# Optimization experiments

Measured on AMD Instinct MI355X. Metric: run time of the kernel, lower is better.

Reference implementation:

```python
import jax, jax.numpy as jnp
import numpy as np

NUM_HEADS = 8
HEAD_DIM = 64
LATENT = NUM_HEADS * HEAD_DIM  # 512
IN_CH = 256


def setup_inputs() -> dict:
    key = jax.random.key(0)
    k1, k2, k3, k4 = jax.random.split(key, 4)
    b, c, h, w = 16, IN_CH, 64, 64
    net = jax.random.normal(k1, (b, c, h, w), dtype=jnp.float32)
    # 1x1 conv weights (out_ch, in_ch); scaled like kaiming-ish init
    w_qkv = jax.random.normal(k2, (3 * LATENT, c), dtype=jnp.float32) / np.sqrt(c)
    w_out = jax.random.normal(k3, (c, LATENT), dtype=jnp.float32) / np.sqrt(LATENT)
    b_out = jax.random.normal(k4, (c,), dtype=jnp.float32) * 0.01
    return {"net": net, "w_qkv": w_qkv, "w_out": w_out, "b_out": b_out}


def reference(net, w_qkv, w_out, b_out):
    b, c, h, w = net.shape
    n = h * w
    # 1x1 conv == channel GEMM: (b, 3L, n)
    qkv = jnp.einsum("bchw,oc->bohw", net, w_qkv).reshape(b, 3, NUM_HEADS, HEAD_DIM, n)
    q, k, v = qkv[:, 0], qkv[:, 1], qkv[:, 2]  # each (b, H, D, n)
    k = jax.nn.softmax(k, axis=-1)  # softmax over spatial tokens
    context = jnp.einsum("bhdn,bhen->bhde", k, v)  # (b, H, D, D)
    out = jnp.einsum("bhde,bhdn->bhen", context, q)  # (b, H, D, n)
    out = out.reshape(b, LATENT, h, w)
    # output 1x1 conv with bias
    out = jnp.einsum("blhw,cl->bchw", out, w_out) + b_out[None, :, None, None]
    return out
```

## Files before the change

### kernel.cpp

```cpp
#include <hip/hip_runtime.h>


typedef unsigned short u16;
typedef unsigned int u32;
typedef __attribute__((ext_vector_type(4))) u16 u16x4;
typedef __attribute__((ext_vector_type(4))) u32 u32x4;
typedef __attribute__((ext_vector_type(4))) float f32x4;
typedef __attribute__((ext_vector_type(8))) short bf16x8;

__device__ __forceinline__ u16 f2bf(float f) {
  union { float f; u32 u; } x; x.f = f;
  u32 r = x.u + 0x7fffu + ((x.u >> 16) & 1u);
  return (u16)(r >> 16);
}

__device__ __forceinline__ void async16(const u16* g, u16* l) {
  __builtin_amdgcn_global_load_lds(
      (const __attribute__((address_space(1))) void*)g,
      (__attribute__((address_space(3))) void*)l, 16, 0, 0);
}

__global__ __launch_bounds__(256) void prep_all(const float* __restrict__ net,
                                                u16* __restrict__ netT,
                                                const float* __restrict__ wqkv,
                                                u16* __restrict__ wkv,
                                                u16* __restrict__ wqTb) {
  __shared__ float t[64][65];
  const int blk = blockIdx.x;
  const int tid = threadIdx.x;
  if (blk < 4096) {
    const int b = blk >> 8, c0 = ((blk >> 6) & 3) * 64, n0 = (blk & 63) * 64;
    const float* ip = net + (size_t)b * 256 * 4096;
    u16* op = netT + (size_t)b * 256 * 4096;
    const int col4 = (tid & 15) * 4, rr0 = tid >> 4;
#pragma unroll
    for (int i = 0; i < 4; ++i) {
      int r = rr0 + i * 16;
      f32x4 v = *(const f32x4*)(ip + (size_t)(c0 + r) * 4096 + n0 + col4);
      t[r][col4 + 0] = v[0]; t[r][col4 + 1] = v[1];
      t[r][col4 + 2] = v[2]; t[r][col4 + 3] = v[3];
    }
    __syncthreads();
    const int c8 = (tid & 7) * 8, nr0 = tid >> 3;
#pragma unroll
    for (int i = 0; i < 2; ++i) {
      int nr = nr0 + i * 32;
      u16 tmp[8];
#pragma unroll
      for (int k = 0; k < 8; ++k) tmp[k] = f2bf(t[c8 + k][nr]);
      *(u32x4*)(op + (size_t)(n0 + nr) * 256 + c0 + c8) = *(const u32x4*)tmp;
    }
  } else if (blk < 4352) {
    const float* w = wqkv + 512 * 256;
    int i = ((blk - 4096) * 256 + tid) * 4;
    f32x4 v = *(const f32x4*)(w + i);
    u16x4 u;
    u[0] = f2bf(v[0]); u[1] = f2bf(v[1]); u[2] = f2bf(v[2]); u[3] = f2bf(v[3]);
    *(u16x4*)(wkv + i) = u;
  } else {
    const int idx = blk - 4352;
    const int c0 = (idx & 3) * 64, r0 = (idx >> 2) * 64;
    const int col4 = (tid & 15) * 4, rr0 = tid >> 4;
#pragma unroll
    for (int i = 0; i < 4; ++i) {
      int r = rr0 + i * 16;
      f32x4 v = *(const f32x4*)(wqkv + (size_t)(r0 + r) * 256 + c0 + col4);
      t[r][col4 + 0] = v[0]; t[r][col4 + 1] = v[1];
      t[r][col4 + 2] = v[2]; t[r][col4 + 3] = v[3];
    }
    __syncthreads();
    const int cc4 = (tid & 15) * 4, nr0 = tid >> 4;
#pragma unroll
    for (int i = 0; i < 4; ++i) {
      int nr = nr0 + i * 16;
      u16x4 u;
      u[0] = f2bf(t[cc4 + 0][nr]); u[1] = f2bf(t[cc4 + 1][nr]);
      u[2] = f2bf(t[cc4 + 2][nr]); u[3] = f2bf(t[cc4 + 3][nr]);
      *(u16x4*)(wqTb + (size_t)(c0 + nr) * 512 + r0 + cc4) = u;
    }
  }
}

__global__ __launch_bounds__(512, 4) void kv_ctx_fused(
    const u16* __restrict__ wkv,
    const u16* __restrict__ netT,
    float* __restrict__ ctxp,
    float* __restrict__ sump) {
  __shared__ __align__(16) u16 Bs[2][8192];
  __shared__ __align__(16) u16 ekL[2][2048];
  __shared__ __align__(16) u16 vL[2][2048];

  const int flat = blockIdx.x;
  const int xcd = flat & 7, inner = flat >> 3;
  const int b = 2 * xcd + (inner >> 5);
  const int h = (inner >> 2) & 7;
  const int s = inner & 3;

  const int tid = threadIdx.x, lane = tid & 63, wid = tid >> 6;
  const int wq = wid & 3, wn = wid >> 2;
  const int lr = lane & 15, lg = lane >> 4;
  const bool isK = (wq < 2);

  bf16x8 af[2][8];
#pragma unroll
  for (int mi = 0; mi < 2; ++mi) {
    const int r = wq * 32 + mi * 16 + lr;
    const int grow = (r < 64) ? h * 64 + r : 512 + h * 64 + (r - 64);
#pragma unroll
    for (int kk = 0; kk < 8; ++kk)
      af[mi][kk] = *(const bf16x8*)(wkv + (size_t)grow * 256 + kk * 32 + lg * 8);
  }

  const u16* Bsrc = netT + ((size_t)b * 4096 + s * 1024) * 256;
  const int srow = tid >> 5;
  const int sslot = tid & 31;
  auto stage = [&](int c, int buf) {
    const u16* src = Bsrc + (size_t)c * 32 * 256;
#pragma unroll
    for (int i = 0; i < 2; ++i) {
      const int row = i * 16 + srow;
      const int scol = ((sslot ^ (row & 7)) * 8);
      async16(src + row * 256 + scol, &Bs[buf][i * 4096 + tid * 8]);
    }
  };

  f32x4 cacc[2] = {};
  f32x4 sacc = {};
  bf16x8 ones8;
#pragma unroll
  for (int j = 0; j < 8; ++j) ((u16*)&ones8)[j] = 0x3F80;

  auto ctx_acc = [&](int q) {
    const int d = wq * 16 + lr;
    bf16x8 ekf = *(const bf16x8*)&ekL[q][d * 32 + ((lg ^ (d & 3)) * 8)];
#pragma unroll
    for (int ei = 0; ei < 2; ++ei) {
      const int e = wn * 32 + ei * 16 + lr;
      bf16x8 vf = *(const bf16x8*)&vL[q][e * 32 + ((lg ^ (e & 3)) * 8)];
      cacc[ei] = __builtin_amdgcn_mfma_f32_16x16x32_bf16(ekf, vf, cacc[ei], 0, 0, 0);
    }
    if (wn == 0)
      sacc = __builtin_amdgcn_mfma_f32_16x16x32_bf16(ekf, ones8, sacc, 0, 0, 0);
  };

  stage(0, 0);
  const int nrow = wn * 16 + lr;

  for (int c = 0; c < 32; ++c) {
    const int p = c & 1;
    __syncthreads();
    if (c + 1 < 32) stage(c + 1, p ^ 1);

    f32x4 kvacc[2] = {};
    __builtin_amdgcn_s_setprio(1);
    if (c > 0) ctx_acc(p ^ 1);
#pragma unroll
    for (int kk = 0; kk < 8; ++kk) {
      bf16x8 bfr = *(const bf16x8*)&Bs[p][nrow * 256 + (((kk * 4 + lg) ^ (nrow & 7)) * 8)];
      kvacc[0] = __builtin_amdgcn_mfma_f32_16x16x32_bf16(af[0][kk], bfr, kvacc[0], 0, 0, 0);
      kvacc[1] = __builtin_amdgcn_mfma_f32_16x16x32_bf16(af[1][kk], bfr, kvacc[1], 0, 0, 0);
    }
    __builtin_amdgcn_s_setprio(0);

    u16* dstL = isK ? ekL[p] : vL[p];
#pragma unroll
    for (int mi = 0; mi < 2; ++mi)
#pragma unroll
      for (int j = 0; j < 4; ++j) {
        float v = kvacc[mi][j];
        if (isK) v = __expf(v);
        const u32 u = __float_as_uint(v);
        const u16 bv = (u16)((u + 0x8000u) >> 16);
        const int dd = (wq & 1) * 32 + mi * 16 + lg * 4 + j;
        dstL[dd * 32 + (((nrow >> 3) ^ (dd & 3)) * 8) + (nrow & 7)] = bv;
      }
  }
  __syncthreads();
  ctx_acc(1);

  float* cp = ctxp + (((size_t)(b * 8 + h) * 4 + s) * 4096);
#pragma unroll
  for (int ei = 0; ei < 2; ++ei)
#pragma unroll
    for (int j = 0; j < 4; ++j) {
      const int d = wq * 16 + lg * 4 + j;
      const int e = wn * 32 + ei * 16 + lr;
      cp[d * 64 + e] = cacc[ei][j];
    }
  if (wn == 0 && lr == 0) {
#pragma unroll
    for (int j = 0; j < 4; ++j)
      sump[((size_t)(b * 8 + h) * 4 + s) * 64 + wq * 16 + lg * 4 + j] = sacc[j];
  }
}

__global__ __launch_bounds__(256) void fold_w2(const float* __restrict__ ctxp,
                                               const float* __restrict__ sump,
                                               const float* __restrict__ wout,
                                               u16* __restrict__ W2) {
  __shared__ float cl[16 * 64];
  __shared__ float sl[16];
  const int bh = blockIdx.x, dq = blockIdx.y;
  const int b = bh >> 3, h = bh & 7;
  const int tid = threadIdx.x;
  f32x4 v4 = {0.f, 0.f, 0.f, 0.f};
#pragma unroll
  for (int ch = 0; ch < 4; ++ch)
    v4 += *(const f32x4*)(ctxp + ((size_t)bh * 4 + ch) * 4096 + dq * 1024 + tid * 4);
  *(f32x4*)&cl[tid * 4] = v4;
  if (tid < 16) {
    float ss = 0.f;
#pragma unroll
    for (int ch = 0; ch < 4; ++ch)
      ss += sump[((size_t)bh * 4 + ch) * 64 + dq * 16 + tid];
    sl[tid] = ss;
  }
  __syncthreads();
  const int c = tid;
  f32x4 wv[16];
  const float* wrow = wout + (size_t)c * 512 + h * 64;
#pragma unroll
  for (int i = 0; i < 16; ++i) wv[i] = *(const f32x4*)(wrow + i * 4);
#pragma unroll
  for (int d = 0; d < 16; ++d) {
    f32x4 s4 = {0.f, 0.f, 0.f, 0.f};
#pragma unroll
    for (int e4 = 0; e4 < 16; ++e4) {
      f32x4 cv = *(const f32x4*)&cl[d * 64 + e4 * 4];
      s4 += wv[e4] * cv;
    }
    const float s = (s4[0] + s4[1] + s4[2] + s4[3]) / sl[d];
    W2[((size_t)b * 256 + c) * 512 + h * 64 + dq * 16 + d] = f2bf(s);
  }
}

template <int LD, int NK, int MODE>
__global__ __launch_bounds__(256) void gemm128(const u16* __restrict__ A,
                                               const u16* __restrict__ B,
                                               size_t aStride, size_t bStride,
                                               void* __restrict__ O0,
                                               const float* __restrict__ bias) {
  __shared__ __align__(16) u16 SM[32768];
  int b, mt, nt;
  if constexpr (MODE == 1) {
    const int flat = blockIdx.x;
    const int xcd = flat & 7, r = flat >> 3;
    b = 2 * xcd + (r >> 6);
    nt = (r & 63) >> 1;
    mt = r & 1;
  } else {
    b = blockIdx.z; mt = blockIdx.y; nt = blockIdx.x;
  }
  const int tid = threadIdx.x, lane = tid & 63, wid = tid >> 6;
  const int wr = wid >> 1, wc = wid & 1, lr = lane & 15, lg = lane >> 4;
  const u16* Ap = A + (size_t)b * aStride + (size_t)mt * 128 * LD;
  const u16* Bp = B + (size_t)b * bStride + (size_t)nt * 128 * LD;

  auto stage = [&](int buf, int ks) {
    const int k0 = ks * 64;
#pragma unroll
    for (int i = 0; i < 4; ++i) {
      const int idx = i * 2048 + tid * 8;
      const int r2 = idx >> 6, c2 = idx & 63;
      async16(Ap + (size_t)r2 * LD + k0 + c2, SM + buf * 8192 + i * 2048 + wid * 512);
      async16(Bp + (size_t)r2 * LD + k0 + c2, SM + 16384 + buf * 8192 + i * 2048 + wid * 512);
    }
  };

  f32x4 acc[4][4] = {};
  stage(0, 0);
  asm volatile("s_waitcnt vmcnt(0)" ::: "memory");
  __syncthreads();
  for (int ks = 0; ks < NK; ++ks) {
    const int buf = ks & 1;
    if (ks + 1 < NK) stage(buf ^ 1, ks + 1);
    const u16* Ab = SM + buf * 8192;
    const u16* Bb = SM + 16384 + buf * 8192;
#pragma unroll
    for (int kk = 0; kk < 2; ++kk) {
      bf16x8 afm[4], bfr[4];
#pragma unroll
      for (int mi = 0; mi < 4; ++mi)
        afm[mi] = *(const bf16x8*)(Ab + (wr * 64 + mi * 16 + lr) * 64 + kk * 32 + lg * 8);
#pragma unroll
      for (int ni = 0; ni < 4; ++ni)
        bfr[ni] = *(const bf16x8*)(Bb + (wc * 64 + ni * 16 + lr) * 64 + kk * 32 + lg * 8);
#pragma unroll
      for (int mi = 0; mi < 4; ++mi)
#pragma unroll
        for (int ni = 0; ni < 4; ++ni)
          acc[mi][ni] = __builtin_amdgcn_mfma_f32_16x16x32_bf16(afm[mi], bfr[ni], acc[mi][ni], 0, 0, 0);
    }
    asm volatile("s_waitcnt vmcnt(0)" ::: "memory");
    __syncthreads();
  }

  if constexpr (MODE == 2) {
    u16* Cs = SM;
#pragma unroll
    for (int mi = 0; mi < 4; ++mi)
#pragma unroll
      for (int ni = 0; ni < 4; ++ni)
#pragma unroll
        for (int j = 0; j < 4; ++j)
          Cs[(wr * 64 + mi * 16 + lg * 4 + j) * 128 + wc * 64 + ni * 16 + lr] =
              f2bf(acc[mi][ni][j]);
    __syncthreads();
    u16* dst = (u16*)O0;
#pragma unroll
    for (int p = 0; p < 8; ++p) {
      const int idx = p * 2048 + tid * 8;
      const int r2 = idx >> 7, cc = idx & 127;
      *(u32x4*)(dst + ((size_t)b * 256 + mt * 128 + r2) * 256 + nt * 128 + cc) =
          *(const u32x4*)(Cs + idx);
    }
  } else {
    float* Cf = (float*)SM;
#pragma unroll
    for (int mi = 0; mi < 4; ++mi)
#pragma unroll
      for (int ni = 0; ni < 4; ++ni)
#pragma unroll
        for (int j = 0; j < 4; ++j) {
          const int row = wr * 64 + mi * 16 + lg * 4 + j;
          Cf[row * 128 + wc * 64 + ni * 16 + lr] = acc[mi][ni][j] + bias[mt * 128 + row];
        }
    __syncthreads();
    float* op = (float*)O0;
#pragma unroll
    for (int p = 0; p < 16; ++p) {
      const int idx = p * 1024 + tid * 4;
      const int r2 = idx >> 7, cc = idx & 127;
      *(f32x4*)(op + ((size_t)b * 256 + mt * 128 + r2) * 4096 + nt * 128 + cc) =
          *(const f32x4*)(Cf + idx);
    }
  }
}

extern "C" void kernel_launch(void* const* d_in, const int* in_sizes, int n_in,
                              void* d_out, int out_size, void* d_ws, size_t ws_size,
                              hipStream_t stream) {
  const float* net  = (const float*)d_in[0];
  const float* wqkv = (const float*)d_in[1];
  const float* wout = (const float*)d_in[2];
  const float* bout = (const float*)d_in[3];
  float* out = (float*)d_out;

  char* ws = (char*)d_ws;
  u16*   netT = (u16*)(ws + 0);
  float* ctxp = (float*)(ws + 33554432);
  float* sump = (float*)(ws + 41943040);
  u16*   W2   = (u16*)(ws + 42074112);
  u16*   W3   = (u16*)(ws + 46268416);
  u16*   wkv  = (u16*)(ws + 48365568);
  u16*   wqTb = (u16*)(ws + 48889856);

  prep_all<<<4384, 256, 0, stream>>>(net, netT, wqkv, wkv, wqTb);
  kv_ctx_fused<<<512, 512, 0, stream>>>(wkv, netT, ctxp, sump);
  fold_w2<<<dim3(128, 4), 256, 0, stream>>>(ctxp, sump, wout, W2);
  gemm128<512, 8, 2><<<dim3(2, 2, 16), 256, 0, stream>>>(
      W2, wqTb, (size_t)256 * 512, 0, W3, nullptr);
  gemm128<256, 4, 1><<<dim3(1024, 1, 1), 256, 0, stream>>>(
      W3, netT, (size_t)256 * 256, (size_t)4096 * 256, out, bout);
}
```

Before: 106.6 us.

## Fuse fold_w2 into kv_ctx_fused via last-block ticket reduction

Removes the separate fold_w2 launch. Each of the four split blocks per (batch, head) takes an atomic ticket after writing its partial context, and the last one reduces the partials and computes the W2 fold in place, reusing shared memory. Ticket counters are zeroed by an extra block in prep_all. This saves a kernel launch and the gap between kernels, at the cost of a tail of serialized fold work in the last-arriving blocks and reliance on threadfence ordering.

```diff
diff --git a/kernel.cpp b/kernel.cpp
--- a/kernel.cpp
+++ b/kernel.cpp
@@ -24,7 +24,8 @@
                                                 u16* __restrict__ netT,
                                                 const float* __restrict__ wqkv,
                                                 u16* __restrict__ wkv,
-                                                u16* __restrict__ wqTb) {
+                                                u16* __restrict__ wqTb,
+                                                int* __restrict__ tickets) {
   __shared__ float t[64][65];
   const int blk = blockIdx.x;
   const int tid = threadIdx.x;
@@ -57,7 +58,7 @@
     u16x4 u;
     u[0] = f2bf(v[0]); u[1] = f2bf(v[1]); u[2] = f2bf(v[2]); u[3] = f2bf(v[3]);
     *(u16x4*)(wkv + i) = u;
-  } else {
+  } else if (blk < 4384) {
     const int idx = blk - 4352;
     const int c0 = (idx & 3) * 64, r0 = (idx >> 2) * 64;
     const int col4 = (tid & 15) * 4, rr0 = tid >> 4;
@@ -78,6 +79,8 @@
       u[2] = f2bf(t[cc4 + 2][nr]); u[3] = f2bf(t[cc4 + 3][nr]);
       *(u16x4*)(wqTb + (size_t)(c0 + nr) * 512 + r0 + cc4) = u;
     }
+  } else {
+    if (tid < 128) tickets[tid] = 0;
   }
 }
 
@@ -85,10 +88,14 @@
     const u16* __restrict__ wkv,
     const u16* __restrict__ netT,
     float* __restrict__ ctxp,
-    float* __restrict__ sump) {
+    float* __restrict__ sump,
+    const float* __restrict__ wout,
+    u16* __restrict__ W2,
+    int* __restrict__ tickets) {
   __shared__ __align__(16) u16 Bs[2][8192];
   __shared__ __align__(16) u16 ekL[2][2048];
   __shared__ __align__(16) u16 vL[2][2048];
+  __shared__ int tks;
 
   const int flat = blockIdx.x;
   const int xcd = flat & 7, inner = flat >> 3;
@@ -178,7 +185,8 @@
   __syncthreads();
   ctx_acc(1);
 
-  float* cp = ctxp + (((size_t)(b * 8 + h) * 4 + s) * 4096);
+  const int bh = b * 8 + h;
+  float* cp = ctxp + (((size_t)bh * 4 + s) * 4096);
 #pragma unroll
   for (int ei = 0; ei < 2; ++ei)
 #pragma unroll
@@ -190,47 +198,49 @@
   if (wn == 0 && lr == 0) {
 #pragma unroll
     for (int j = 0; j < 4; ++j)
-      sump[((size_t)(b * 8 + h) * 4 + s) * 64 + wq * 16 + lg * 4 + j] = sacc[j];
-  }
-}
-
-__global__ __launch_bounds__(256) void fold_w2(const float* __restrict__ ctxp,
-                                               const float* __restrict__ sump,
-                                               const float* __restrict__ wout,
-                                               u16* __restrict__ W2) {
-  __shared__ float cl[16 * 64];
-  __shared__ float sl[16];
-  const int bh = blockIdx.x, dq = blockIdx.y;
-  const int b = bh >> 3, h = bh & 7;
-  const int tid = threadIdx.x;
-  f32x4 v4 = {0.f, 0.f, 0.f, 0.f};
-#pragma unroll
-  for (int ch = 0; ch < 4; ++ch)
-    v4 += *(const f32x4*)(ctxp + ((size_t)bh * 4 + ch) * 4096 + dq * 1024 + tid * 4);
-  *(f32x4*)&cl[tid * 4] = v4;
-  if (tid < 16) {
-    float ss = 0.f;
-#pragma unroll
-    for (int ch = 0; ch < 4; ++ch)
-      ss += sump[((size_t)bh * 4 + ch) * 64 + dq * 16 + tid];
-    sl[tid] = ss;
-  }
+      sump[((size_t)bh * 4 + s) * 64 + wq * 16 + lg * 4 + j] = sacc[j];
+  }
+
+  __threadfence();
+  if (tid == 0) tks = atomicAdd(&tickets[bh], 1);
   __syncthreads();
-  const int c = tid;
-  f32x4 wv[16];
-  const float* wrow = wout + (size_t)c * 512 + h * 64;
-#pragma unroll
-  for (int i = 0; i < 16; ++i) wv[i] = *(const f32x4*)(wrow + i * 4);
-#pragma unroll
-  for (int d = 0; d < 16; ++d) {
-    f32x4 s4 = {0.f, 0.f, 0.f, 0.f};
-#pragma unroll
-    for (int e4 = 0; e4 < 16; ++e4) {
-      f32x4 cv = *(const f32x4*)&cl[d * 64 + e4 * 4];
-      s4 += wv[e4] * cv;
-    }
-    const float s = (s4[0] + s4[1] + s4[2] + s4[3]) / sl[d];
-    W2[((size_t)b * 256 + c) * 512 + h * 64 + dq * 16 + d] = f2bf(s);
+  if (tks == 3) {
+    __threadfence();
+    float* scr = (float*)Bs;
+    float* clS = scr;
+    float* slS = scr + 2048;
+    const int half = tid >> 8, t2 = tid & 255;
+    f32x4 wv[16];
+    const float* wrow = wout + (size_t)t2 * 512 + h * 64;
+#pragma unroll
+    for (int i = 0; i < 16; ++i) wv[i] = *(const f32x4*)(wrow + i * 4);
+#pragma unroll
+    for (int dqp = 0; dqp < 2; ++dqp) {
+      const int dq = dqp * 2 + half;
+      f32x4 v4 = {0.f, 0.f, 0.f, 0.f};
+#pragma unroll
+      for (int ch = 0; ch < 4; ++ch)
+        v4 += *(const f32x4*)(ctxp + ((size_t)bh * 4 + ch) * 4096 + dq * 1024 + t2 * 4);
+      *(f32x4*)&clS[half * 1024 + t2 * 4] = v4;
+      if (t2 < 16) {
+        float ss = 0.f;
+#pragma unroll
+        for (int ch = 0; ch < 4; ++ch)
+          ss += sump[((size_t)bh * 4 + ch) * 64 + dq * 16 + t2];
+        slS[half * 16 + t2] = ss;
+      }
+      __syncthreads();
+#pragma unroll
+      for (int d = 0; d < 16; ++d) {
+        f32x4 s4 = {0.f, 0.f, 0.f, 0.f};
+#pragma unroll
+        for (int e4 = 0; e4 < 16; ++e4)
+          s4 += wv[e4] * *(const f32x4*)&clS[half * 1024 + d * 64 + e4 * 4];
+        const float sv = (s4[0] + s4[1] + s4[2] + s4[3]) / slS[half * 16 + d];
+        W2[((size_t)b * 256 + t2) * 512 + h * 64 + dq * 16 + d] = f2bf(sv);
+      }
+      __syncthreads();
+    }
   }
 }
 
@@ -354,10 +364,10 @@
   u16*   W3   = (u16*)(ws + 46268416);
   u16*   wkv  = (u16*)(ws + 48365568);
   u16*   wqTb = (u16*)(ws + 48889856);
-
-  prep_all<<<4384, 256, 0, stream>>>(net, netT, wqkv, wkv, wqTb);
-  kv_ctx_fused<<<512, 512, 0, stream>>>(wkv, netT, ctxp, sump);
-  fold_w2<<<dim3(128, 4), 256, 0, stream>>>(ctxp, sump, wout, W2);
+  int*   tick = (int*)(ws + 49152000);
+
+  prep_all<<<4385, 256, 0, stream>>>(net, netT, wqkv, wkv, wqTb, tick);
+  kv_ctx_fused<<<512, 512, 0, stream>>>(wkv, netT, ctxp, sump, wout, W2, tick);
   gemm128<512, 8, 2><<<dim3(2, 2, 16), 256, 0, stream>>>(
       W2, wqTb, (size_t)256 * 512, 0, W3, nullptr);
   gemm128<256, 4, 1><<<dim3(1024, 1, 1), 256, 0, stream>>>(
```

After: 232.7 us. 118% more time.

## Process two heads per block in kv_ctx_fused to reuse staged input tiles

Applied to the files above, without the earlier changes.

Each block of the fused K/V-context kernel now computes two heads over half as many spatial tokens (8 spatial splits instead of 4), so one staged netT tile feeds both heads' K and V projections. Each warp owns a full 64-wide context row block, and the fold kernel now sums 8 partials instead of 4. The goal is to halve the netT traffic per head and raise MFMA work per LDS load. In exchange, LDS use and accumulator registers go up, the ctxp workspace doubles, and the pipeline has only 16 chunks per block.

```diff
diff --git a/kernel.cpp b/kernel.cpp
--- a/kernel.cpp
+++ b/kernel.cpp
@@ -87,31 +87,34 @@
     float* __restrict__ ctxp,
     float* __restrict__ sump) {
   __shared__ __align__(16) u16 Bs[2][8192];
-  __shared__ __align__(16) u16 ekL[2][2048];
-  __shared__ __align__(16) u16 vL[2][2048];
+  __shared__ __align__(16) u16 ekL[2][2][2048];
+  __shared__ __align__(16) u16 vL[2][2][2048];
 
   const int flat = blockIdx.x;
   const int xcd = flat & 7, inner = flat >> 3;
   const int b = 2 * xcd + (inner >> 5);
-  const int h = (inner >> 2) & 7;
-  const int s = inner & 3;
+  const int hp = (inner >> 3) & 3;
+  const int s = inner & 7;
 
   const int tid = threadIdx.x, lane = tid & 63, wid = tid >> 6;
-  const int wq = wid & 3, wn = wid >> 2;
   const int lr = lane & 15, lg = lane >> 4;
-  const bool isK = (wq < 2);
+  const int head_loc = wid >> 2;
+  const int h = hp * 2 + head_loc;
+  const bool isK = ((wid >> 1) & 1) == 0;
+  const int rbase = (wid & 1) * 32;
+  const int w4 = wid & 3;
 
   bf16x8 af[2][8];
 #pragma unroll
   for (int mi = 0; mi < 2; ++mi) {
-    const int r = wq * 32 + mi * 16 + lr;
-    const int grow = (r < 64) ? h * 64 + r : 512 + h * 64 + (r - 64);
+    const int rl = rbase + mi * 16 + lr;
+    const int grow = isK ? (h * 64 + rl) : (512 + h * 64 + rl);
 #pragma unroll
     for (int kk = 0; kk < 8; ++kk)
       af[mi][kk] = *(const bf16x8*)(wkv + (size_t)grow * 256 + kk * 32 + lg * 8);
   }
 
-  const u16* Bsrc = netT + ((size_t)b * 4096 + s * 1024) * 256;
+  const u16* Bsrc = netT + ((size_t)b * 4096 + s * 512) * 256;
   const int srow = tid >> 5;
   const int sslot = tid & 31;
   auto stage = [&](int c, int buf) {
@@ -124,73 +127,79 @@
     }
   };
 
-  f32x4 cacc[2] = {};
+  f32x4 cacc[4] = {};
   f32x4 sacc = {};
   bf16x8 ones8;
 #pragma unroll
   for (int j = 0; j < 8; ++j) ((u16*)&ones8)[j] = 0x3F80;
 
   auto ctx_acc = [&](int q) {
-    const int d = wq * 16 + lr;
-    bf16x8 ekf = *(const bf16x8*)&ekL[q][d * 32 + ((lg ^ (d & 3)) * 8)];
-#pragma unroll
-    for (int ei = 0; ei < 2; ++ei) {
-      const int e = wn * 32 + ei * 16 + lr;
-      bf16x8 vf = *(const bf16x8*)&vL[q][e * 32 + ((lg ^ (e & 3)) * 8)];
+    const int d = w4 * 16 + lr;
+    bf16x8 ekf = *(const bf16x8*)&ekL[head_loc][q][d * 32 + ((lg ^ (d & 3)) * 8)];
+#pragma unroll
+    for (int ei = 0; ei < 4; ++ei) {
+      const int e = ei * 16 + lr;
+      bf16x8 vf = *(const bf16x8*)&vL[head_loc][q][e * 32 + ((lg ^ (e & 3)) * 8)];
       cacc[ei] = __builtin_amdgcn_mfma_f32_16x16x32_bf16(ekf, vf, cacc[ei], 0, 0, 0);
     }
-    if (wn == 0)
-      sacc = __builtin_amdgcn_mfma_f32_16x16x32_bf16(ekf, ones8, sacc, 0, 0, 0);
+    sacc = __builtin_amdgcn_mfma_f32_16x16x32_bf16(ekf, ones8, sacc, 0, 0, 0);
   };
 
   stage(0, 0);
-  const int nrow = wn * 16 + lr;
-
-  for (int c = 0; c < 32; ++c) {
+
+  for (int c = 0; c < 16; ++c) {
     const int p = c & 1;
     __syncthreads();
-    if (c + 1 < 32) stage(c + 1, p ^ 1);
-
-    f32x4 kvacc[2] = {};
+    if (c + 1 < 16) stage(c + 1, p ^ 1);
+
+    f32x4 kvacc[2][2] = {};
     __builtin_amdgcn_s_setprio(1);
     if (c > 0) ctx_acc(p ^ 1);
 #pragma unroll
     for (int kk = 0; kk < 8; ++kk) {
-      bf16x8 bfr = *(const bf16x8*)&Bs[p][nrow * 256 + (((kk * 4 + lg) ^ (nrow & 7)) * 8)];
-      kvacc[0] = __builtin_amdgcn_mfma_f32_16x16x32_bf16(af[0][kk], bfr, kvacc[0], 0, 0, 0);
-      kvacc[1] = __builtin_amdgcn_mfma_f32_16x16x32_bf16(af[1][kk], bfr, kvacc[1], 0, 0, 0);
+      bf16x8 bf0 = *(const bf16x8*)&Bs[p][lr * 256 + (((kk * 4 + lg) ^ (lr & 7)) * 8)];
+      bf16x8 bf1 = *(const bf16x8*)&Bs[p][(16 + lr) * 256 + (((kk * 4 + lg) ^ (lr & 7)) * 8)];
+#pragma unroll
+      for (int mi = 0; mi < 2; ++mi) {
+        kvacc[mi][0] = __builtin_amdgcn_mfma_f32_16x16x32_bf16(af[mi][kk], bf0, kvacc[mi][0], 0, 0, 0);
+        kvacc[mi][1] = __builtin_amdgcn_mfma_f32_16x16x32_bf16(af[mi][kk], bf1, kvacc[mi][1], 0, 0, 0);
+      }
     }
     __builtin_amdgcn_s_setprio(0);
 
-    u16* dstL = isK ? ekL[p] : vL[p];
+    u16* dstL = isK ? ekL[head_loc][p] : vL[head_loc][p];
 #pragma unroll
     for (int mi = 0; mi < 2; ++mi)
 #pragma unroll
-      for (int j = 0; j < 4; ++j) {
-        float v = kvacc[mi][j];
-        if (isK) v = __expf(v);
-        const u32 u = __float_as_uint(v);
-        const u16 bv = (u16)((u + 0x8000u) >> 16);
-        const int dd = (wq & 1) * 32 + mi * 16 + lg * 4 + j;
-        dstL[dd * 32 + (((nrow >> 3) ^ (dd & 3)) * 8) + (nrow & 7)] = bv;
-      }
+      for (int nj = 0; nj < 2; ++nj)
+#pragma unroll
+        for (int j = 0; j < 4; ++j) {
+          float v = kvacc[mi][nj][j];
+          if (isK) v = __expf(v);
+          const u32 u = __float_as_uint(v);
+          const u16 bv = (u16)((u + 0x8000u) >> 16);
+          const int dd = rbase + mi * 16 + lg * 4 + j;
+          const int n = nj * 16 + lr;
+          dstL[dd * 32 + (((n >> 3) ^ (dd & 3)) * 8) + (n & 7)] = bv;
+        }
   }
   __syncthreads();
   ctx_acc(1);
 
-  float* cp = ctxp + (((size_t)(b * 8 + h) * 4 + s) * 4096);
-#pragma unroll
-  for (int ei = 0; ei < 2; ++ei)
+  const int bh = b * 8 + h;
+  float* cp = ctxp + (((size_t)bh * 8 + s) * 4096);
+#pragma unroll
+  for (int ei = 0; ei < 4; ++ei)
 #pragma unroll
     for (int j = 0; j < 4; ++j) {
-      const int d = wq * 16 + lg * 4 + j;
-      const int e = wn * 32 + ei * 16 + lr;
+      const int d = w4 * 16 + lg * 4 + j;
+      const int e = ei * 16 + lr;
       cp[d * 64 + e] = cacc[ei][j];
     }
-  if (wn == 0 && lr == 0) {
+  if (lr == 0) {
 #pragma unroll
     for (int j = 0; j < 4; ++j)
-      sump[((size_t)(b * 8 + h) * 4 + s) * 64 + wq * 16 + lg * 4 + j] = sacc[j];
+      sump[((size_t)bh * 8 + s) * 64 + w4 * 16 + lg * 4 + j] = sacc[j];
   }
 }
 
@@ -205,14 +214,14 @@
   const int tid = threadIdx.x;
   f32x4 v4 = {0.f, 0.f, 0.f, 0.f};
 #pragma unroll
-  for (int ch = 0; ch < 4; ++ch)
-    v4 += *(const f32x4*)(ctxp + ((size_t)bh * 4 + ch) * 4096 + dq * 1024 + tid * 4);
+  for (int ch = 0; ch < 8; ++ch)
+    v4 += *(const f32x4*)(ctxp + ((size_t)bh * 8 + ch) * 4096 + dq * 1024 + tid * 4);
   *(f32x4*)&cl[tid * 4] = v4;
   if (tid < 16) {
     float ss = 0.f;
 #pragma unroll
-    for (int ch = 0; ch < 4; ++ch)
-      ss += sump[((size_t)bh * 4 + ch) * 64 + dq * 16 + tid];
+    for (int ch = 0; ch < 8; ++ch)
+      ss += sump[((size_t)bh * 8 + ch) * 64 + dq * 16 + tid];
     sl[tid] = ss;
   }
   __syncthreads();
@@ -349,11 +358,11 @@
   char* ws = (char*)d_ws;
   u16*   netT = (u16*)(ws + 0);
   float* ctxp = (float*)(ws + 33554432);
-  float* sump = (float*)(ws + 41943040);
-  u16*   W2   = (u16*)(ws + 42074112);
-  u16*   W3   = (u16*)(ws + 46268416);
-  u16*   wkv  = (u16*)(ws + 48365568);
-  u16*   wqTb = (u16*)(ws + 48889856);
+  float* sump = (float*)(ws + 50331648);
+  u16*   W2   = (u16*)(ws + 50593792);
+  u16*   W3   = (u16*)(ws + 54788096);
+  u16*   wkv  = (u16*)(ws + 56885248);
+  u16*   wqTb = (u16*)(ws + 57409536);
 
   prep_all<<<4384, 256, 0, stream>>>(net, netT, wqkv, wkv, wqTb);
   kv_ctx_fused<<<512, 512, 0, stream>>>(wkv, netT, ctxp, sump);
```

Measured after the change: 110.1 us. 1.03x slower.
